# Optimization experiments

Hardware: AMD Instinct MI355X
Metric: run time of the kernel (lower is better)

## Reference

```python
import jax, jax.numpy as jnp
import numpy as np

EPS = 1e-8  # torch F.cosine_similarity eps


def setup_inputs() -> dict:
    key = jax.random.key(0)
    k1, k2 = jax.random.split(key)
    n, d = 8192, 128
    embeddings = jax.random.normal(k1, (n, d), dtype=jnp.float32)
    labels = jax.random.randint(k2, (n,), 0, 256, dtype=jnp.int64)
    return {"embeddings": embeddings, "labels": labels}


def reference(embeddings, labels):
    # Miner(mode='hardest', use_cosine_dist=True), is_front=None, is_ref=None.
    # get_cosine_dist_matrix: 1 - cos_sim over all pairs == normalize once + GEMM.
    n = embeddings.shape[0]
    norms = jnp.linalg.norm(embeddings, axis=1, keepdims=True)
    en = embeddings / jnp.maximum(norms, EPS)          # [n, d]
    dist = 1.0 - en @ en.T                             # [n, n] cosine distance

    same = labels[:, None] == labels[None, :]          # [n, n]
    diag = jnp.eye(n, dtype=bool)
    pos_mask = same & ~diag                            # diagonal filled with -inf in torch
    neg_mask = ~same                                   # diagonal is same-label -> excluded

    pos_d = jnp.where(pos_mask, dist, -jnp.inf)
    neg_d = jnp.where(neg_mask, dist, jnp.inf)

    hardest_pos_dist = jnp.max(pos_d, axis=1)
    hardest_pos_inds = jnp.argmax(pos_d, axis=1)       # first max, matches torch .max(dim=1)
    hardest_neg_dist = jnp.min(neg_d, axis=1)
    hardest_neg_inds = jnp.argmin(neg_d, axis=1)

    anchors = jnp.arange(n)
    triplets = jnp.column_stack((anchors, hardest_pos_inds, hardest_neg_inds))  # [n, 3]
    return triplets, hardest_pos_dist, hardest_neg_dist
```

## Files before the change

### kernel.cpp

```cpp
#include <hip/hip_runtime.h>
#include <hip/hip_bf16.h>
#include <math.h>

#define N 8192
#define D 128
#define MARGIN 4e-5f
#define FLAGBIT 0x80000000
#define IDXMASK 0x1FFF

typedef __attribute__((ext_vector_type(8))) short short8;
typedef __attribute__((ext_vector_type(4))) float f32x4;
typedef unsigned long long u64;

__device__ __forceinline__ unsigned int ordered_u32(float f) {
    unsigned int b = __float_as_uint(f);
    return (b & 0x80000000u) ? ~b : (b | 0x80000000u);
}
__device__ __forceinline__ float ordered_inv(unsigned int u) {
    unsigned int b = (u & 0x80000000u) ? (u & 0x7FFFFFFFu) : ~u;
    return __uint_as_float(b);
}

__global__ __launch_bounds__(256) void prep_kernel(const float* __restrict__ e,
                                                   __hip_bfloat16* __restrict__ hi,
                                                   __hip_bfloat16* __restrict__ lo,
                                                   float* __restrict__ nrm,
                                                   int* __restrict__ counter,
                                                   u64* __restrict__ pos_key,
                                                   u64* __restrict__ neg_key) {
    if (blockIdx.x == 0 && threadIdx.x == 0) *counter = 0;
    int row  = blockIdx.x * 4 + (threadIdx.x >> 6);
    int lane = threadIdx.x & 63;
    if (lane == 0) { pos_key[row] = ~0ull; neg_key[row] = ~0ull; }
    float2 v = ((const float2*)(e + (size_t)row * D))[lane];
    float s = v.x * v.x + v.y * v.y;
    #pragma unroll
    for (int m = 1; m < 64; m <<= 1) s += __shfl_xor(s, m, 64);
    float nr = sqrtf(s);
    if (lane == 0) nrm[row] = nr;
    float rn = 1.0f / fmaxf(nr, 1e-8f);
    float e0 = v.x * rn, e1 = v.y * rn;
    __hip_bfloat16 h0 = __float2bfloat16(e0);
    __hip_bfloat16 h1 = __float2bfloat16(e1);
    __hip_bfloat16 l0 = __float2bfloat16(e0 - __bfloat162float(h0));
    __hip_bfloat16 l1 = __float2bfloat16(e1 - __bfloat162float(h1));
    ushort2 hh, ll;
    hh.x = *(unsigned short*)&h0; hh.y = *(unsigned short*)&h1;
    ll.x = *(unsigned short*)&l0; ll.y = *(unsigned short*)&l1;
    ((ushort2*)hi)[row * 64 + lane] = hh;
    ((ushort2*)lo)[row * 64 + lane] = ll;
}

__global__ __launch_bounds__(256, 2) void mine_kernel(
    const __hip_bfloat16* __restrict__ hi, const __hip_bfloat16* __restrict__ lo,
    const int* __restrict__ labels, int4* __restrict__ partials) {

    __shared__ short Ahi[128 * 128];
    __shared__ short Alo[128 * 128];
    __shared__ int   lab_sh[1024];

    const int tid = threadIdx.x;
    const int l = tid & 63;
    const int w = tid >> 6;
    const int ihalf = w >> 1, jhalf = w & 1;
    const int i0 = blockIdx.x * 128;
    const int j0base = blockIdx.y * 1024;
    const int lq = l >> 4;
    const int ln = l & 15;

    {
        const int arr = tid >> 7;
        const int r = tid & 127;
        const __hip_bfloat16* src = (arr ? lo : hi) + (size_t)(i0 + r) * D;
        short* dst = (arr ? Alo : Ahi) + r * 128;
        #pragma unroll
        for (int c = 0; c < 16; ++c) {
            short8 vv = *(const short8*)(src + c * 8);
            *(short8*)(dst + ((c ^ (r & 7)) * 8)) = vv;
        }
    }
    {
        int4 lv = ((const int4*)(labels + j0base))[tid];
        ((int4*)lab_sh)[tid] = lv;
    }
    __syncthreads();

    int li[16];
    int ibase[4];
    #pragma unroll
    for (int mt = 0; mt < 4; ++mt) ibase[mt] = i0 + ihalf * 64 + mt * 16 + lq * 4;
    #pragma unroll
    for (int s = 0; s < 16; ++s) li[s] = labels[ibase[s >> 2] + (s & 3)];

    float posv[16], negv[16];
    int   posi[16], negi[16];
    #pragma unroll
    for (int s = 0; s < 16; ++s) {
        posv[s] = -INFINITY; posi[s] = 0;
        negv[s] =  INFINITY; negi[s] = 0;
    }

    const short* hs = (const short*)hi;
    const short* ls = (const short*)lo;

    for (int jt = 0; jt < 8; ++jt) {
        const int j0 = j0base + jt * 128;
        const int jrow0 = j0 + jhalf * 64 + ln;

        f32x4 acc[4][4];
        #pragma unroll
        for (int mt = 0; mt < 4; ++mt)
            #pragma unroll
            for (int nt = 0; nt < 4; ++nt) acc[mt][nt] = (f32x4){0.f, 0.f, 0.f, 0.f};

        #pragma unroll 2
        for (int kc = 0; kc < 4; ++kc) {
            short8 bh4[4], bl4[4];
            #pragma unroll
            for (int nt = 0; nt < 4; ++nt) {
                size_t off = (size_t)(jrow0 + nt * 16) * D + kc * 32 + lq * 8;
                bh4[nt] = *(const short8*)(hs + off);
                bl4[nt] = *(const short8*)(ls + off);
            }
            #pragma unroll
            for (int mt = 0; mt < 4; ++mt) {
                int r = ihalf * 64 + mt * 16 + ln;
                int slot = (kc * 4 + lq) ^ (ln & 7);
                short8 ah = *(short8*)(Ahi + r * 128 + slot * 8);
                short8 al = *(short8*)(Alo + r * 128 + slot * 8);
                #pragma unroll
                for (int nt = 0; nt < 4; ++nt) {
                    acc[mt][nt] = __builtin_amdgcn_mfma_f32_16x16x32_bf16(ah, bh4[nt], acc[mt][nt], 0, 0, 0);
                    acc[mt][nt] = __builtin_amdgcn_mfma_f32_16x16x32_bf16(ah, bl4[nt], acc[mt][nt], 0, 0, 0);
                    acc[mt][nt] = __builtin_amdgcn_mfma_f32_16x16x32_bf16(al, bh4[nt], acc[mt][nt], 0, 0, 0);
                }
            }
        }

        int jv[4], lj[4];
        #pragma unroll
        for (int nt = 0; nt < 4; ++nt) {
            jv[nt] = jrow0 + nt * 16;
            lj[nt] = lab_sh[jv[nt] - j0base];
        }
        #pragma unroll
        for (int nt = 0; nt < 4; ++nt) {
            #pragma unroll
            for (int mt = 0; mt < 4; ++mt) {
                #pragma unroll
                for (int r = 0; r < 4; ++r) {
                    const int s = mt * 4 + r;
                    float dd = 1.0f - acc[mt][nt][r];
                    bool same = (lj[nt] == li[s]);
                    bool self = (jv[nt] == ibase[mt] + r);
                    if (same) {
                        if (!self) {
                            bool nr = fabsf(dd - posv[s]) < MARGIN;
                            if (dd > posv[s]) { posv[s] = dd; posi[s] = jv[nt] | (nr ? FLAGBIT : 0); }
                            else if (nr) posi[s] |= FLAGBIT;
                        }
                    } else {
                        bool nr = fabsf(dd - negv[s]) < MARGIN;
                        if (dd < negv[s]) { negv[s] = dd; negi[s] = jv[nt] | (nr ? FLAGBIT : 0); }
                        else if (nr) negi[s] |= FLAGBIT;
                    }
                }
            }
        }
    }

    #pragma unroll
    for (int s = 0; s < 16; ++s) {
        float pv = posv[s]; int pif = posi[s];
        float nv = negv[s]; int nif = negi[s];
        #pragma unroll
        for (int off = 1; off < 16; off <<= 1) {
            float opv = __shfl_xor(pv, off, 64); int opif = __shfl_xor(pif, off, 64);
            float onv = __shfl_xor(nv, off, 64); int onif = __shfl_xor(nif, off, 64);
            bool pnr = fabsf(opv - pv) < MARGIN;
            bool nnr = fabsf(onv - nv) < MARGIN;
            if (opv > pv) { pv = opv; pif = opif; }
            if (pnr) pif |= FLAGBIT;
            if (onv < nv) { nv = onv; nif = onif; }
            if (nnr) nif |= FLAGBIT;
        }
        if (ln == s) {
            int ii = ibase[s >> 2] + (s & 3);
            partials[ii * 16 + blockIdx.y * 2 + jhalf] =
                make_int4(__float_as_int(pv), pif, __float_as_int(nv), nif);
        }
    }
}

__global__ __launch_bounds__(256) void combine_kernel(
    const int4* __restrict__ partials, float* __restrict__ out,
    int* __restrict__ list, int* __restrict__ counter) {
    int tid = threadIdx.x;
    int a = blockIdx.x * 64 + (tid >> 2);
    int q = tid & 3;
    float pv = -INFINITY; int pif = 0;
    float nv =  INFINITY; int nif = 0;
    #pragma unroll
    for (int s = 0; s < 4; ++s) {
        int4 p = partials[a * 16 + q * 4 + s];
        float dv = __int_as_float(p.x);
        bool nr = fabsf(dv - pv) < MARGIN;
        if (dv > pv) { pv = dv; pif = p.y; }
        if (nr) pif |= FLAGBIT;
        float ev = __int_as_float(p.z);
        bool nr2 = fabsf(ev - nv) < MARGIN;
        if (ev < nv) { nv = ev; nif = p.w; }
        if (nr2) nif |= FLAGBIT;
    }
    #pragma unroll
    for (int off = 1; off < 4; off <<= 1) {
        float opv = __shfl_xor(pv, off, 64); int opif = __shfl_xor(pif, off, 64);
        float onv = __shfl_xor(nv, off, 64); int onif = __shfl_xor(nif, off, 64);
        bool pnr = fabsf(opv - pv) < MARGIN;
        bool nnr = fabsf(onv - nv) < MARGIN;
        int opidx = opif & IDXMASK, pidx = pif & IDXMASK;
        if (opv > pv || (opv == pv && opidx < pidx)) { pv = opv; pif = opif; }
        if (pnr) pif |= FLAGBIT;
        int onidx = onif & IDXMASK, nidx = nif & IDXMASK;
        if (onv < nv || (onv == nv && onidx < nidx)) { nv = onv; nif = onif; }
        if (nnr) nif |= FLAGBIT;
    }
    if (q == 0) {
        out[a * 3 + 0] = (float)a;
        out[a * 3 + 1] = (float)(pif & IDXMASK);
        out[a * 3 + 2] = (float)(nif & IDXMASK);
        out[3 * N + a] = pv;
        out[4 * N + a] = nv;
        if ((pif | nif) & FLAGBIT) {
            int k = atomicAdd(counter, 1);
            list[k] = a;
        }
    }
}

__global__ __launch_bounds__(256) void cleanup1_kernel(
    const float* __restrict__ e, const int* __restrict__ labels,
    const float* __restrict__ nrm, const int* __restrict__ list,
    const int* __restrict__ counter,
    u64* __restrict__ pos_key, u64* __restrict__ neg_key) {
    __shared__ float enr[128];
    __shared__ u64 redp[4], redn[4];
    const int tid = threadIdx.x;
    const int lane = tid & 63, w = tid >> 6;
    const int cnt = *counter;
    const int j = blockIdx.y * 256 + tid;

    for (int slot = blockIdx.x; slot < cnt; slot += gridDim.x) {
        __syncthreads();
        const int row = list[slot];
        if (tid < 128) enr[tid] = e[(size_t)row * D + tid] / fmaxf(nrm[row], 1e-8f);
        __syncthreads();
        const int lr = labels[row];

        const float4* ej = (const float4*)(e + (size_t)j * D);
        float s0 = 0.f, s1 = 0.f, s2 = 0.f, s3 = 0.f;
        #pragma unroll
        for (int c = 0; c < 32; c += 4) {
            float4 v0 = ej[c], v1 = ej[c + 1], v2 = ej[c + 2], v3 = ej[c + 3];
            s0 = fmaf(v0.x, enr[4*c   ], fmaf(v0.y, enr[4*c+ 1], fmaf(v0.z, enr[4*c+ 2], fmaf(v0.w, enr[4*c+ 3], s0))));
            s1 = fmaf(v1.x, enr[4*c+ 4], fmaf(v1.y, enr[4*c+ 5], fmaf(v1.z, enr[4*c+ 6], fmaf(v1.w, enr[4*c+ 7], s1))));
            s2 = fmaf(v2.x, enr[4*c+ 8], fmaf(v2.y, enr[4*c+ 9], fmaf(v2.z, enr[4*c+10], fmaf(v2.w, enr[4*c+11], s2))));
            s3 = fmaf(v3.x, enr[4*c+12], fmaf(v3.y, enr[4*c+13], fmaf(v3.z, enr[4*c+14], fmaf(v3.w, enr[4*c+15], s3))));
        }
        float dd = 1.0f - ((s0 + s1) + (s2 + s3)) / fmaxf(nrm[j], 1e-8f);

        u64 pk = ~0ull, nk = ~0ull;
        if (j != row) {
            unsigned int u = ordered_u32(dd);
            if (labels[j] == lr) pk = ((u64)(~u) << 32) | (unsigned int)j;
            else                 nk = ((u64)( u) << 32) | (unsigned int)j;
        }
        #pragma unroll
        for (int off = 1; off < 64; off <<= 1) {
            u64 op = __shfl_xor(pk, off, 64); if (op < pk) pk = op;
            u64 on = __shfl_xor(nk, off, 64); if (on < nk) nk = on;
        }
        if (lane == 0) { redp[w] = pk; redn[w] = nk; }
        __syncthreads();
        if (tid == 0) {
            #pragma unroll
            for (int q = 1; q < 4; ++q) {
                if (redp[q] < pk) pk = redp[q];
                if (redn[q] < nk) nk = redn[q];
            }
            if (pk != ~0ull) atomicMin(&pos_key[row], pk);
            if (nk != ~0ull) atomicMin(&neg_key[row], nk);
        }
    }
}

__global__ __launch_bounds__(256) void cleanup2_kernel(
    const u64* __restrict__ pos_key, const u64* __restrict__ neg_key,
    const int* __restrict__ list, const int* __restrict__ counter,
    float* __restrict__ out) {
    int idx = blockIdx.x * 256 + threadIdx.x;
    int cnt = *counter;
    if (idx >= cnt) return;
    int row = list[idx];
    u64 pk = pos_key[row], nk = neg_key[row];
    if (pk != ~0ull) {
        unsigned int u = ~(unsigned int)(pk >> 32);
        out[row * 3 + 1] = (float)(unsigned int)(pk & 0xFFFFFFFFu);
        out[3 * N + row] = ordered_inv(u);
    }
    if (nk != ~0ull) {
        unsigned int u = (unsigned int)(nk >> 32);
        out[row * 3 + 2] = (float)(unsigned int)(nk & 0xFFFFFFFFu);
        out[4 * N + row] = ordered_inv(u);
    }
}

extern "C" void kernel_launch(void* const* d_in, const int* in_sizes, int n_in,
                              void* d_out, int out_size, void* d_ws, size_t ws_size,
                              hipStream_t stream) {
    const float* e      = (const float*)d_in[0];
    const int*   labels = (const int*)d_in[1];
    float* out = (float*)d_out;

    char* wsb = (char*)d_ws;
    __hip_bfloat16* hi = (__hip_bfloat16*)wsb;
    __hip_bfloat16* lo = hi + (size_t)N * D;
    float* nrm   = (float*)(wsb + 4u * 1024 * 1024);
    int4*  parts = (int4*)(wsb + 4u * 1024 * 1024 + 65536);
    int*   list  = (int*)(wsb + 7u * 1024 * 1024);
    int*   cnt   = (int*)(wsb + 7u * 1024 * 1024 + 65536);
    u64*   pkey  = (u64*)(wsb + 7u * 1024 * 1024 + 131072);
    u64*   nkey  = (u64*)(wsb + 7u * 1024 * 1024 + 196608);

    prep_kernel<<<N / 4, 256, 0, stream>>>(e, hi, lo, nrm, cnt, pkey, nkey);
    mine_kernel<<<dim3(N / 128, 8), 256, 0, stream>>>(hi, lo, labels, parts);
    combine_kernel<<<N / 64, 256, 0, stream>>>(parts, out, list, cnt);
    cleanup1_kernel<<<dim3(256, 32), 256, 0, stream>>>(e, labels, nrm, list, cnt, pkey, nkey);
    cleanup2_kernel<<<N / 256, 256, 0, stream>>>(pkey, nkey, list, cnt, out);
}
```

Baseline: 178.0 us.

## Double-buffer B fragment global loads across flattened jt/kc loop

Flattens the j-tile and k-chunk loops into one 32-step loop and prefetches the next step's hi/lo B fragments from global memory into a second register buffer while the MFMAs for the current step run. The first prefetch is issued before the block barrier. This is meant to hide global load latency behind MFMA work and to keep the pipeline going across tile boundaries, including during the epilogue. It costs extra VGPRs for the second buffer and adds a conditional epilogue inside the loop, which may lower occupancy or cause spills.

```diff
diff --git a/kernel.cpp b/kernel.cpp
--- a/kernel.cpp
+++ b/kernel.cpp
@@ -83,6 +83,24 @@
         int4 lv = ((const int4*)(labels + j0base))[tid];
         ((int4*)lab_sh)[tid] = lv;
     }
+
+    const short* __restrict__ hs = (const short*)hi;
+    const short* __restrict__ ls = (const short*)lo;
+
+    short8 bH[2][4], bL[2][4];
+    const size_t lanoff = (size_t)(j0base + jhalf * 64 + ln) * D + lq * 8;
+
+#define ISSUE_B(rr, buf) do {                                                   \
+        const int jt_ = (rr) >> 2, kc_ = (rr) & 3;                              \
+        const size_t base_ = lanoff + (size_t)jt_ * 128 * D + kc_ * 32;         \
+        _Pragma("unroll")                                                       \
+        for (int nt_ = 0; nt_ < 4; ++nt_) {                                     \
+            bH[buf][nt_] = *(const short8*)(hs + base_ + (size_t)nt_ * 16 * D); \
+            bL[buf][nt_] = *(const short8*)(ls + base_ + (size_t)nt_ * 16 * D); \
+        }                                                                       \
+    } while (0)
+
+    ISSUE_B(0, 0);
     __syncthreads();
 
     int li[16];
@@ -100,74 +118,72 @@
         negv[s] =  INFINITY; negi[s] = 0;
     }
 
-    const short* hs = (const short*)hi;
-    const short* ls = (const short*)lo;
-
-    for (int jt = 0; jt < 8; ++jt) {
-        const int j0 = j0base + jt * 128;
-        const int jrow0 = j0 + jhalf * 64 + ln;
-
-        f32x4 acc[4][4];
-        #pragma unroll
-        for (int mt = 0; mt < 4; ++mt)
-            #pragma unroll
-            for (int nt = 0; nt < 4; ++nt) acc[mt][nt] = (f32x4){0.f, 0.f, 0.f, 0.f};
-
-        #pragma unroll 2
-        for (int kc = 0; kc < 4; ++kc) {
-            short8 bh4[4], bl4[4];
+    f32x4 acc[4][4];
+    #pragma unroll
+    for (int mt = 0; mt < 4; ++mt)
+        #pragma unroll
+        for (int nt = 0; nt < 4; ++nt) acc[mt][nt] = (f32x4){0.f, 0.f, 0.f, 0.f};
+
+    #pragma unroll 2
+    for (int r = 0; r < 32; ++r) {
+        const int cur = r & 1;
+        if (r < 31) ISSUE_B(r + 1, cur ^ 1);
+        const int kc = r & 3;
+
+        #pragma unroll
+        for (int mt = 0; mt < 4; ++mt) {
+            int row = ihalf * 64 + mt * 16 + ln;
+            int slot = (kc * 4 + lq) ^ (ln & 7);
+            short8 ah = *(short8*)(Ahi + row * 128 + slot * 8);
+            short8 al = *(short8*)(Alo + row * 128 + slot * 8);
             #pragma unroll
             for (int nt = 0; nt < 4; ++nt) {
-                size_t off = (size_t)(jrow0 + nt * 16) * D + kc * 32 + lq * 8;
-                bh4[nt] = *(const short8*)(hs + off);
-                bl4[nt] = *(const short8*)(ls + off);
+                acc[mt][nt] = __builtin_amdgcn_mfma_f32_16x16x32_bf16(ah, bH[cur][nt], acc[mt][nt], 0, 0, 0);
+                acc[mt][nt] = __builtin_amdgcn_mfma_f32_16x16x32_bf16(ah, bL[cur][nt], acc[mt][nt], 0, 0, 0);
+                acc[mt][nt] = __builtin_amdgcn_mfma_f32_16x16x32_bf16(al, bH[cur][nt], acc[mt][nt], 0, 0, 0);
             }
-            #pragma unroll
-            for (int mt = 0; mt < 4; ++mt) {
-                int r = ihalf * 64 + mt * 16 + ln;
-                int slot = (kc * 4 + lq) ^ (ln & 7);
-                short8 ah = *(short8*)(Ahi + r * 128 + slot * 8);
-                short8 al = *(short8*)(Alo + r * 128 + slot * 8);
+        }
+
+        if (kc == 3) {
+            const int j0 = j0base + (r >> 2) * 128;
+            const int jrow0 = j0 + jhalf * 64 + ln;
+            int jv[4], lj[4];
+            #pragma unroll
+            for (int nt = 0; nt < 4; ++nt) {
+                jv[nt] = jrow0 + nt * 16;
+                lj[nt] = lab_sh[jv[nt] - j0base];
+            }
+            #pragma unroll
+            for (int nt = 0; nt < 4; ++nt) {
                 #pragma unroll
-                for (int nt = 0; nt < 4; ++nt) {
-                    acc[mt][nt] = __builtin_amdgcn_mfma_f32_16x16x32_bf16(ah, bh4[nt], acc[mt][nt], 0, 0, 0);
-                    acc[mt][nt] = __builtin_amdgcn_mfma_f32_16x16x32_bf16(ah, bl4[nt], acc[mt][nt], 0, 0, 0);
-                    acc[mt][nt] = __builtin_amdgcn_mfma_f32_16x16x32_bf16(al, bh4[nt], acc[mt][nt], 0, 0, 0);
-                }
-            }
-        }
-
-        int jv[4], lj[4];
-        #pragma unroll
-        for (int nt = 0; nt < 4; ++nt) {
-            jv[nt] = jrow0 + nt * 16;
-            lj[nt] = lab_sh[jv[nt] - j0base];
-        }
-        #pragma unroll
-        for (int nt = 0; nt < 4; ++nt) {
-            #pragma unroll
-            for (int mt = 0; mt < 4; ++mt) {
-                #pragma unroll
-                for (int r = 0; r < 4; ++r) {
-                    const int s = mt * 4 + r;
-                    float dd = 1.0f - acc[mt][nt][r];
-                    bool same = (lj[nt] == li[s]);
-                    bool self = (jv[nt] == ibase[mt] + r);
-                    if (same) {
-                        if (!self) {
-                            bool nr = fabsf(dd - posv[s]) < MARGIN;
-                            if (dd > posv[s]) { posv[s] = dd; posi[s] = jv[nt] | (nr ? FLAGBIT : 0); }
-                            else if (nr) posi[s] |= FLAGBIT;
+                for (int mt = 0; mt < 4; ++mt) {
+                    #pragma unroll
+                    for (int rr = 0; rr < 4; ++rr) {
+                        const int s = mt * 4 + rr;
+                        float dd = 1.0f - acc[mt][nt][rr];
+                        bool same = (lj[nt] == li[s]);
+                        bool self = (jv[nt] == ibase[mt] + rr);
+                        if (same) {
+                            if (!self) {
+                                bool nr = fabsf(dd - posv[s]) < MARGIN;
+                                if (dd > posv[s]) { posv[s] = dd; posi[s] = jv[nt] | (nr ? FLAGBIT : 0); }
+                                else if (nr) posi[s] |= FLAGBIT;
+                            }
+                        } else {
+                            bool nr = fabsf(dd - negv[s]) < MARGIN;
+                            if (dd < negv[s]) { negv[s] = dd; negi[s] = jv[nt] | (nr ? FLAGBIT : 0); }
+                            else if (nr) negi[s] |= FLAGBIT;
                         }
-                    } else {
-                        bool nr = fabsf(dd - negv[s]) < MARGIN;
-                        if (dd < negv[s]) { negv[s] = dd; negi[s] = jv[nt] | (nr ? FLAGBIT : 0); }
-                        else if (nr) negi[s] |= FLAGBIT;
                     }
                 }
             }
-        }
-    }
+            #pragma unroll
+            for (int mt = 0; mt < 4; ++mt)
+                #pragma unroll
+                for (int nt = 0; nt < 4; ++nt) acc[mt][nt] = (f32x4){0.f, 0.f, 0.f, 0.f};
+        }
+    }
+#undef ISSUE_B
 
     #pragma unroll
     for (int s = 0; s < 16; ++s) {
```

Result: slower. 181.7 us (+2.1%).
